# Kernel optimization log

Hardware: AMD Instinct MI355X
Metric: run time of the kernel (lower is better)

The kernel has to match this reference:

```python
import jax, jax.numpy as jnp
import numpy as np

B, T, D_IN, D_OUT, N_FILT, MAX_T = 4, 2048, 512, 512, 24, 2048


def _hankel_filters(max_t: int, k: int) -> np.ndarray:
    # Z_{ij} = 2 / ((i+j)^3 - (i+j)), 1-indexed; top-|eig| eigenvectors
    idx = np.arange(1, max_t + 1, dtype=np.float64)
    ij = idx[None, :] + idx[:, None]
    Z = 2.0 / (ij ** 3 - ij)
    w, v = np.linalg.eigh(Z)
    top = np.argsort(-np.abs(w))[:k]
    return v[:, top].astype(np.float32)  # (max_t, k)


def setup_inputs() -> dict:
    key = jax.random.key(0)
    kx, km = jax.random.split(key)
    x = jax.random.normal(kx, (B, T, D_IN), dtype=jnp.float32)
    filters = jnp.asarray(_hankel_filters(MAX_T, N_FILT))  # (MAX_T, N)
    # nn.Linear weight is (d_out, d_in); stacked -> (N, d_out, d_in)
    scale = 1.0 / np.sqrt(D_IN)
    M_weights = jax.random.uniform(km, (N_FILT, D_OUT, D_IN), dtype=jnp.float32,
                                   minval=-scale, maxval=scale)
    return {"x": x, "filters": filters, "M_weights": M_weights}


def reference(x, filters, M_weights):
    Tlen = x.shape[1]
    phi = filters[:Tlen]                       # (T, N)
    phi_e = phi[None, :, :, None]              # (1, T, N, 1)
    weighted = phi_e * x[:, :, None, :]        # (B, T, N, D_in)
    csum = jnp.cumsum(weighted, axis=1)        # causal cumulative projection
    # per-filter rectangular projection: (B,T,N,f) x (N,o,f) -> (B,T,N,o)
    modulated = jnp.einsum('btnf,nof->btno', csum, M_weights)
    return (phi_e * modulated).sum(axis=2)     # (B, T, D_out)
```

## Files before the change

### kernel.cpp

```cpp
#include <hip/hip_runtime.h>
#include <stdint.h>

#define BQ 4
#define TT 2048
#define DF 512
#define DOUT 512
#define NF 24
#define CHF 8

typedef __attribute__((ext_vector_type(8))) short short8;
typedef __attribute__((ext_vector_type(4))) float f32x4;

typedef __attribute__((address_space(3))) uint8_t       lds_u8;
typedef __attribute__((address_space(1))) const uint8_t glb_u8;

__device__ __forceinline__ float bf2f(unsigned short u) {
    union { unsigned int i; float f; } v; v.i = ((unsigned int)u) << 16; return v.f;
}
__device__ __forceinline__ unsigned short f2bf(float f) {
    union { float f; unsigned int i; } v; v.f = f;
    unsigned int r = v.i + 0x7FFFu + ((v.i >> 16) & 1u);
    return (unsigned short)(r >> 16);
}
__device__ __forceinline__ float lo16f(unsigned int u) { return __uint_as_float(u << 16); }
__device__ __forceinline__ float hi16f(unsigned int u) { return __uint_as_float(u & 0xffff0000u); }

__device__ __forceinline__ int plaus16(unsigned int h) {
    unsigned int e = (h >> 7) & 0xffu;
    return (e >= 97u && e <= 141u) || ((h & 0x7fffu) == 0u);
}

__global__ void k_detect(const unsigned int* __restrict__ X, int* __restrict__ flag)
{
    const int lane = threadIdx.x;
    int cnt = 0;
#pragma unroll
    for (int i = 0; i < 4; ++i) {
        unsigned int w = X[lane * 4 + i];
        cnt += (plaus16(w >> 16) && plaus16(w & 0xffffu)) ? 1 : 0;
    }
    for (int off = 32; off > 0; off >>= 1) cnt += __shfl_down(cnt, off);
    if (lane == 0) *flag = (cnt < 180) ? 1 : 0;
}

__global__ __launch_bounds__(256) void k_convf(
    const void* __restrict__ src, float* __restrict__ dst,
    const int* __restrict__ flag, int n)
{
    const int isf32 = *flag;
    int i = blockIdx.x * 256 + threadIdx.x;
    const int stride = gridDim.x * 256;
    for (; i < n; i += stride)
        dst[i] = isf32 ? ((const float*)src)[i]
                       : bf2f(((const unsigned short*)src)[i]);
}

__global__ __launch_bounds__(256) void k_prep(
    const void* __restrict__ X, const void* __restrict__ Mw,
    const void* __restrict__ Fil,
    unsigned short* __restrict__ Xbf, unsigned short* __restrict__ Mbf,
    float* __restrict__ Fw, int n4x, int n4m, int n4f)
{
    __shared__ int sflag;
    const int tid = threadIdx.x;
    if (tid < 64) {
        int cnt = 0;
        const unsigned int* Xu = (const unsigned int*)X;
#pragma unroll
        for (int i = 0; i < 4; ++i) {
            unsigned int wd = Xu[tid * 4 + i];
            cnt += (plaus16(wd >> 16) && plaus16(wd & 0xffffu)) ? 1 : 0;
        }
        for (int off = 32; off > 0; off >>= 1) cnt += __shfl_down(cnt, off);
        if (tid == 0) sflag = (cnt < 180) ? 1 : 0;
    }
    __syncthreads();
    const int isf32 = sflag;

    const int total = n4x + n4m + n4f;
    for (int i = blockIdx.x * 256 + tid; i < total; i += gridDim.x * 256) {
        if (i < n4x) {
            ushort4 o;
            if (isf32) {
                float4 v = ((const float4*)X)[i];
                o.x = f2bf(v.x); o.y = f2bf(v.y); o.z = f2bf(v.z); o.w = f2bf(v.w);
            } else {
                o = ((const ushort4*)X)[i];
            }
            ((ushort4*)Xbf)[i] = o;
        } else if (i < n4x + n4m) {
            const int j = i - n4x;
            ushort4 o;
            if (isf32) {
                float4 v = ((const float4*)Mw)[j];
                o.x = f2bf(v.x); o.y = f2bf(v.y); o.z = f2bf(v.z); o.w = f2bf(v.w);
            } else {
                o = ((const ushort4*)Mw)[j];
            }
            ((ushort4*)Mbf)[j] = o;
        } else {
            const int j = i - n4x - n4m;
            if (isf32) {
                ((float4*)Fw)[j] = ((const float4*)Fil)[j];
            } else {
                ushort4 u = ((const ushort4*)Fil)[j];
                ((float4*)Fw)[j] = make_float4(bf2f(u.x), bf2f(u.y),
                                               bf2f(u.z), bf2f(u.w));
            }
        }
    }
}

__global__ __launch_bounds__(256, 3) void k_gemm_ns(
    const unsigned short* __restrict__ X,
    const unsigned short* __restrict__ Mw,
    const float* __restrict__ Fw,
    float* __restrict__ Cs,
    float* __restrict__ Out,
    int r0)
{
    __shared__ unsigned short sAB[2 * 6144];
    __shared__ float sPhi2[NF * 64];

    const int tid  = threadIdx.x;
    const int lane = tid & 63;
    const int w    = tid >> 6;
    const int wm   = w & 1, wn = w >> 1;
    const int tm   = blockIdx.x;
    const int on0  = blockIdx.y * 128;
    const int rowL = tm * 64;
    const int rowG = r0 + rowL;

    for (int idx = tid; idx < NF * 64; idx += 256) {
        int n = idx >> 6, rr2 = idx & 63;
        sPhi2[idx] = Fw[((rowG + rr2) & (TT - 1)) * NF + n];
    }

    const unsigned short* Ag = X + (size_t)rowG * DF;

    auto stage = [&](int m) {
        const int n = m >> 4, kt = m & 15;
        lds_u8* base = (lds_u8*)sAB + (m & 1) * 12288;
        {
            const int c = w * 64 + lane;
            const int r = c >> 2, qs = c & 3;
            const int qg = qs ^ ((r >> 1) & 3);
            __builtin_amdgcn_global_load_lds(
                (const glb_u8*)(Ag + (size_t)r * DF + kt * 32 + qg * 8),
                base + (w * 64) * 16, 16, 0, 0);
        }
        const unsigned short* Bg = Mw + (size_t)n * DOUT * DF + (size_t)on0 * DF;
#pragma unroll
        for (int i = 0; i < 2; ++i) {
            const int cbase = i * 256 + w * 64;
            const int c = cbase + lane;
            const int r = c >> 2, qs = c & 3;
            const int qg = qs ^ ((r >> 1) & 3);
            __builtin_amdgcn_global_load_lds(
                (const glb_u8*)(Bg + (size_t)r * DF + kt * 32 + qg * 8),
                base + 4096 + cbase * 16, 16, 0, 0);
        }
    };

    f32x4 acc[2][4], Bacc[2][4];
#pragma unroll
    for (int i = 0; i < 2; i++)
#pragma unroll
        for (int j = 0; j < 4; j++) {
            acc[i][j]  = (f32x4){0.f, 0.f, 0.f, 0.f};
            Bacc[i][j] = (f32x4){0.f, 0.f, 0.f, 0.f};
        }

    stage(0);
    __syncthreads();

    const int lr  = lane & 15;
    const int q   = lane >> 4;
    const int qsw = (q ^ ((lr >> 1) & 3)) * 8;

    for (int m = 0; m < NF * 16; ++m) {
        if (m + 1 < NF * 16) stage(m + 1);

        const unsigned short* sAc = sAB + (m & 1) * 6144;
        const unsigned short* sBc = sAc + 2048;
        short8 a[2], b[4];
#pragma unroll
        for (int i = 0; i < 2; i++)
            a[i] = *(const short8*)&sAc[(wm * 32 + i * 16 + lr) * 32 + qsw];
#pragma unroll
        for (int j = 0; j < 4; j++)
            b[j] = *(const short8*)&sBc[(wn * 64 + j * 16 + lr) * 32 + qsw];
#pragma unroll
        for (int i = 0; i < 2; i++)
#pragma unroll
            for (int j = 0; j < 4; j++)
                acc[i][j] = __builtin_amdgcn_mfma_f32_16x16x32_bf16(
                    a[i], b[j], acc[i][j], 0, 0, 0);

        if ((m & 15) == 15) {
            const int n = m >> 4;
#pragma unroll
            for (int i = 0; i < 2; i++) {
                const int rbase = wm * 32 + i * 16 + q * 4;
                float ph0 = sPhi2[n * 64 + rbase + 0];
                float ph1 = sPhi2[n * 64 + rbase + 1];
                float ph2 = sPhi2[n * 64 + rbase + 2];
                float ph3 = sPhi2[n * 64 + rbase + 3];
#pragma unroll
                for (int j = 0; j < 4; j++) {
                    float z0 = acc[i][j][0] * ph0;
                    float z1 = acc[i][j][1] * ph1;
                    float z2 = acc[i][j][2] * ph2;
                    float z3 = acc[i][j][3] * ph3;
                    float p0 = z0, p1 = p0 + z1, p2 = p1 + z2, p3 = p2 + z3;
                    float t  = __shfl_xor(p3, 16);
                    float off = (q & 1) ? t : 0.f;
                    Bacc[i][j][0] += ph0 * (off + p0);
                    Bacc[i][j][1] += ph1 * (off + p1);
                    Bacc[i][j][2] += ph2 * (off + p2);
                    Bacc[i][j][3] += ph3 * (off + p3);
                    if (q & 1) {
                        int ch  = (rowL >> 3) + wm * 4 + i * 2 + (q >> 1);
                        int col = on0 + wn * 64 + j * 16 + lr;
                        Cs[((size_t)ch * NF + n) * 512 + col] = off + p3;
                    }
                    acc[i][j] = (f32x4){0.f, 0.f, 0.f, 0.f};
                }
            }
        }
        __syncthreads();
    }

#pragma unroll
    for (int i = 0; i < 2; i++)
#pragma unroll
        for (int j = 0; j < 4; j++)
#pragma unroll
            for (int r = 0; r < 4; r++) {
                int row = rowG + wm * 32 + i * 16 + q * 4 + r;
                Out[(size_t)row * DOUT + on0 + wn * 64 + j * 16 + lr] =
                    Bacc[i][j][r];
            }
}

__global__ __launch_bounds__(256, 8) void k_apply(
    float* __restrict__ Out, const float* __restrict__ Cs,
    const float* __restrict__ Fw, int r0)
{
    __shared__ float sP2[CHF * NF];
    const int c = blockIdx.x, tid = threadIdx.x;
    const int t0g = r0 + c * CHF;
    if (tid < CHF * NF)
        sP2[tid] = Fw[((t0g + tid / NF) & (TT - 1)) * NF + (tid % NF)];
    __syncthreads();

    const int col2 = tid * 2;
    float2 a[CHF];
#pragma unroll
    for (int t = 0; t < CHF; ++t) a[t] = make_float2(0.f, 0.f);
    const float* cb = Cs + (size_t)c * NF * 512 + col2;
#pragma unroll 6
    for (int n = 0; n < NF; ++n) {
        float2 g = *(const float2*)(cb + (size_t)n * 512);
#pragma unroll
        for (int t = 0; t < CHF; ++t) {
            float ph = sP2[t * NF + n];
            a[t].x += ph * g.x; a[t].y += ph * g.y;
        }
    }
#pragma unroll
    for (int t = 0; t < CHF; ++t) {
        float2* po = (float2*)&Out[(size_t)(t0g + t) * DOUT + col2];
        float2 o = *po;
        *po = make_float2(o.x + a[t].x, o.y + a[t].y);
    }
}

__global__ __launch_bounds__(256, 2) void k_gemm(
    const void* __restrict__ Xv, const void* __restrict__ Mv,
    const void* __restrict__ Fv, const int* __restrict__ flag,
    unsigned short* __restrict__ Z, int r0, int o0, int W)
{
    __shared__ unsigned short sA[128 * 32];
    __shared__ unsigned short sB[128 * 32];
    __shared__ unsigned short sC[128 * 136];
    __shared__ float sPhi[128];

    const int isf32 = *flag;
    const int tid  = threadIdx.x;
    const int lane = tid & 63;
    const int w    = tid >> 6;
    const int wm   = w & 1, wn = w >> 1;
    const int tm   = blockIdx.x;
    const int on0  = o0 + blockIdx.y * 128;
    const int n    = blockIdx.z;

    const int rowg0 = r0 + tm * 128;
    if (tid < 128) {
        int t = (rowg0 + tid) & (TT - 1);
        sPhi[tid] = isf32 ? ((const float*)Fv)[t * NF + n]
                          : bf2f(((const unsigned short*)Fv)[t * NF + n]);
    }

    const unsigned short* Ah = (const unsigned short*)Xv + (size_t)rowg0 * DF;
    const unsigned short* Bh = (const unsigned short*)Mv +
        (size_t)n * DOUT * DF + (size_t)on0 * DF;
    const float* Af = (const float*)Xv + (size_t)rowg0 * DF;
    const float* Bf = (const float*)Mv + (size_t)n * DOUT * DF + (size_t)on0 * DF;

    f32x4 acc[4][4];
#pragma unroll
    for (int i = 0; i < 4; i++)
#pragma unroll
        for (int j = 0; j < 4; j++) acc[i][j] = (f32x4){0.f, 0.f, 0.f, 0.f};

    for (int kt = 0; kt < DF / 32; ++kt) {
        __syncthreads();
        if (!isf32) {
            const unsigned short* Ak = Ah + kt * 32;
            const unsigned short* Bk = Bh + kt * 32;
#pragma unroll
            for (int i = 0; i < 2; ++i) {
                const int c = i * 256 + tid;
                const int r = c >> 2, cc = (c & 3) * 8;
                *(short8*)&sA[r * 32 + cc] = *(const short8*)(Ak + (size_t)r * DF + cc);
                *(short8*)&sB[r * 32 + cc] = *(const short8*)(Bk + (size_t)r * DF + cc);
            }
        } else {
            const float* Ak = Af + kt * 32;
            const float* Bk = Bf + kt * 32;
#pragma unroll
            for (int i = 0; i < 2; ++i) {
                const int c = i * 256 + tid;
                const int r = c >> 2, cc = (c & 3) * 8;
                float4 a0 = *(const float4*)(Ak + (size_t)r * DF + cc);
                float4 a1 = *(const float4*)(Ak + (size_t)r * DF + cc + 4);
                float4 b0 = *(const float4*)(Bk + (size_t)r * DF + cc);
                float4 b1 = *(const float4*)(Bk + (size_t)r * DF + cc + 4);
                short8 sa, sb;
                sa[0]=(short)f2bf(a0.x); sa[1]=(short)f2bf(a0.y);
                sa[2]=(short)f2bf(a0.z); sa[3]=(short)f2bf(a0.w);
                sa[4]=(short)f2bf(a1.x); sa[5]=(short)f2bf(a1.y);
                sa[6]=(short)f2bf(a1.z); sa[7]=(short)f2bf(a1.w);
                sb[0]=(short)f2bf(b0.x); sb[1]=(short)f2bf(b0.y);
                sb[2]=(short)f2bf(b0.z); sb[3]=(short)f2bf(b0.w);
                sb[4]=(short)f2bf(b1.x); sb[5]=(short)f2bf(b1.y);
                sb[6]=(short)f2bf(b1.z); sb[7]=(short)f2bf(b1.w);
                *(short8*)&sA[r * 32 + cc] = sa;
                *(short8*)&sB[r * 32 + cc] = sb;
            }
        }
        __syncthreads();

        const int lr = lane & 15;
        const int lk = (lane >> 4) * 8;
        short8 a[4], b[4];
#pragma unroll
        for (int i = 0; i < 4; i++)
            a[i] = *(const short8*)&sA[(wm * 64 + i * 16 + lr) * 32 + lk];
#pragma unroll
        for (int j = 0; j < 4; j++)
            b[j] = *(const short8*)&sB[(wn * 64 + j * 16 + lr) * 32 + lk];
#pragma unroll
        for (int i = 0; i < 4; i++)
#pragma unroll
            for (int j = 0; j < 4; j++)
                acc[i][j] = __builtin_amdgcn_mfma_f32_16x16x32_bf16(
                    a[i], b[j], acc[i][j], 0, 0, 0);
    }

    const int rb = (lane >> 4) * 4;
#pragma unroll
    for (int i = 0; i < 4; i++)
#pragma unroll
        for (int j = 0; j < 4; j++)
#pragma unroll
            for (int r = 0; r < 4; r++) {
                int row = wm * 64 + i * 16 + rb + r;
                sC[row * 136 + wn * 64 + j * 16 + (lane & 15)] =
                    f2bf(acc[i][j][r] * sPhi[row]);
            }
    __syncthreads();
#pragma unroll
    for (int it = 0; it < 8; ++it) {
        int row = it * 16 + (tid >> 4);
        int col = (tid & 15) * 8;
        uint4 v = *(const uint4*)&sC[row * 136 + col];
        *(uint4*)&Z[((size_t)(tm * 128 + row) * NF + n) * W + (on0 - o0) + col] = v;
    }
}

__global__ __launch_bounds__(256, 2) void k_csum(
    const unsigned short* __restrict__ Z, float* __restrict__ Cs,
    int W, int CHs)
{
    const int c = blockIdx.x, n = blockIdx.y, tid = threadIdx.x;
    const unsigned short* p = Z + ((size_t)(c * CHs) * NF + n) * W + tid * 2;
    float sx = 0.f, sy = 0.f;
#pragma unroll 8
    for (int t = 0; t < CHs; ++t) {
        unsigned int u = *(const unsigned int*)(p + (size_t)t * NF * W);
        sx += lo16f(u);
        sy += hi16f(u);
    }
    float2* q = (float2*)&Cs[((size_t)c * NF + n) * W + tid * 2];
    *q = make_float2(sx, sy);
}

__global__ __launch_bounds__(256, 4) void k_prefix(
    float* __restrict__ Cs, float* __restrict__ Gc,
    int W, int rr, int nch, int nbat)
{
    __shared__ float2 sPart[4][64];
    const int tid  = threadIdx.x;
    const int wv   = tid >> 6, lane = tid & 63;
    const int obw  = W >> 7;
    const int perB = NF * obw;
    const int gw   = blockIdx.x;
    const int b    = gw / perB;
    const int rest = gw % perB;
    const int n    = rest / obw;
    const int ob   = rest % obw;
    const int opair = ob * 64 + lane;

    float* base = Cs + (size_t)b * nch * NF * W + (size_t)n * W + opair * 2;
    const size_t cstride = (size_t)NF * W;
    const int Q  = nch >> 2;
    const int c0 = wv * Q;
    const int end = c0 + Q;

    float sx = 0.f, sy = 0.f;
    for (int c = c0; c < end; ++c) {
        float2 v = *(const float2*)(base + (size_t)c * cstride);
        sx += v.x; sy += v.y;
    }
    sPart[wv][lane] = make_float2(sx, sy);
    __syncthreads();

    float cx = 0.f, cy = 0.f;
    if (nbat == 1 && rr != 0 && Gc) {
        float2 gv = *(const float2*)&Gc[(size_t)n * DOUT + opair * 2];
        cx = gv.x; cy = gv.y;
    }
    for (int w2 = 0; w2 < wv; ++w2) {
        float2 p = sPart[w2][lane];
        cx += p.x; cy += p.y;
    }

    int c = c0;
    if (Q >= 16) {
        float2 v[8], nx[8];
#pragma unroll
        for (int k = 0; k < 8; ++k)
            v[k] = *(float2*)(base + (size_t)(c + k) * cstride);
        for (; c + 16 <= end; c += 8) {
#pragma unroll
            for (int k = 0; k < 8; ++k)
                nx[k] = *(float2*)(base + (size_t)(c + 8 + k) * cstride);
#pragma unroll
            for (int k = 0; k < 8; ++k) {
                float2* p = (float2*)(base + (size_t)(c + k) * cstride);
                float2 t = v[k];
                *p = make_float2(cx, cy);
                cx += t.x; cy += t.y;
                v[k] = nx[k];
            }
        }
#pragma unroll
        for (int k = 0; k < 8; ++k) {
            float2* p = (float2*)(base + (size_t)(c + k) * cstride);
            float2 t = v[k];
            *p = make_float2(cx, cy);
            cx += t.x; cy += t.y;
        }
        c += 8;
    }
    for (; c < end; ++c) {
        float2* p = (float2*)(base + (size_t)c * cstride);
        float2 t = *p;
        *p = make_float2(cx, cy);
        cx += t.x; cy += t.y;
    }

    if (nbat == 1 && wv == 3 && Gc)
        *(float2*)&Gc[(size_t)n * DOUT + opair * 2] = make_float2(cx, cy);
}

#define JLIST(F) F(0) F(1) F(2) F(3) F(4) F(5)

__global__ __launch_bounds__(256, 8) void k_scan(
    const unsigned short* __restrict__ Z, const float* __restrict__ Cs,
    const float* __restrict__ Fw, float* __restrict__ Out,
    int r0, int o0, int W, int CHs)
{
    __shared__ float sPhi[32 * NF];
    __shared__ float2 sP[4][8][64];
    const int cg = blockIdx.x, tid = threadIdx.x;
    const int g = tid >> 6, op = tid & 63;
    const int ng0 = g * 6;
    const int c2  = (blockIdx.y * 64 + op) * 2;
    const int act = (c2 + 2 <= W);
    const int c2u = act ? c2 : (W - 2);
    const int t0g = r0 + cg * CHs;
    const int t0 = t0g & (TT - 1);
    for (int i = tid; i < CHs * NF; i += 256)
        sPhi[i] = Fw[(t0 + i / NF) * NF + (i % NF)];
    __syncthreads();

#define DECLG(j) float gx##j, gy##j;
    JLIST(DECLG)
#define INITG2(j) { float2 v = *(const float2*)&Cs[((size_t)cg * NF + ng0 + j) * W + c2u]; \
                    gx##j = v.x; gy##j = v.y; }
    JLIST(INITG2)

    const unsigned short* zp = Z + ((size_t)cg * CHs * NF + ng0) * W + c2u;
    float* outb = Out + (size_t)t0g * DOUT + o0 + c2;
    for (int tb = 0; tb < CHs; tb += 8) {
#pragma unroll
        for (int tt = 0; tt < 8; ++tt) {
            float ax = 0.f, ay = 0.f;
            const float* php = &sPhi[(tb + tt) * NF + ng0];
#define UPDG2(j) { unsigned int u = *(const unsigned int*)(zp + (size_t)j * W); \
                   gx##j += lo16f(u); gy##j += hi16f(u); \
                   float ph = php[j]; ax += ph * gx##j; ay += ph * gy##j; }
            JLIST(UPDG2)
            sP[g][tt][op] = make_float2(ax, ay);
            zp += (size_t)NF * W;
        }
        __syncthreads();
#pragma unroll
        for (int k = 0; k < 2; ++k) {
            const int tt = g * 2 + k;
            float2 p0 = sP[0][tt][op], p1 = sP[1][tt][op],
                   p2 = sP[2][tt][op], p3 = sP[3][tt][op];
            if (act)
                *(float2*)(outb + (size_t)(tb + tt) * DOUT) =
                    make_float2(p0.x + p1.x + p2.x + p3.x,
                                p0.y + p1.y + p2.y + p3.y);
        }
        __syncthreads();
    }
}

extern "C" void kernel_launch(void* const* d_in, const int* in_sizes, int n_in,
                              void* d_out, int out_size, void* d_ws, size_t ws_size,
                              hipStream_t stream)
{
    const void* X = d_in[0]; const void* Fil = d_in[1]; const void* Mw = d_in[2];
    for (int i = 0; i < n_in && i < 3; ++i) {
        if (in_sizes[i] == BQ * TT * DF)        X   = d_in[i];
        else if (in_sizes[i] == TT * NF)        Fil = d_in[i];
        else if (in_sizes[i] == NF * DOUT * DF) Mw  = d_in[i];
    }
    float* Out = (float*)d_out;

    const size_t offF = 256;
    const size_t nbF  = (size_t)TT * NF * 4;
    const size_t off0 = offF + nbF;
    const size_t nbX  = (size_t)BQ * TT * DF * 2;
    const size_t nbM  = (size_t)NF * DOUT * DF * 2;
    const size_t nbGc = (size_t)NF * DOUT * 4;

    int* flag = (int*)d_ws;
    float* Fw = (float*)((char*)d_ws + offF);

    const int n4x = BQ * TT * DF / 4;
    const int n4m = NF * DOUT * DF / 4;
    const int n4f = TT * NF / 4;

    {
        const size_t csB = (size_t)(BQ * TT / CHF) * NF * 512 * 4;
        if (off0 + nbX + nbM + csB <= ws_size) {
            unsigned short* Xbf = (unsigned short*)((char*)d_ws + off0);
            unsigned short* Mbf = (unsigned short*)((char*)Xbf + nbX);
            float* Cs = (float*)((char*)Mbf + nbM);

            hipLaunchKernelGGL(k_prep, dim3(2048), dim3(256), 0, stream,
                               X, Mw, Fil, Xbf, Mbf, Fw, n4x, n4m, n4f);
            hipLaunchKernelGGL(k_gemm_ns, dim3(BQ * TT / 64, 4), dim3(256),
                               0, stream, Xbf, Mbf, Fw, Cs, Out, 0);
            hipLaunchKernelGGL(k_prefix, dim3(BQ * NF * 4), dim3(256),
                               0, stream, Cs, (float*)nullptr, 512, 0,
                               TT / CHF, BQ);
            hipLaunchKernelGGL(k_apply, dim3(BQ * TT / CHF), dim3(256),
                               0, stream, Out, Cs, Fw, 0);
            return;
        }
    }

    {
        const size_t csB = (size_t)(TT / CHF) * NF * 512 * 4;
        if (off0 + nbX + nbM + csB <= ws_size) {
            unsigned short* Xbf = (unsigned short*)((char*)d_ws + off0);
            unsigned short* Mbf = (unsigned short*)((char*)Xbf + nbX);
            float* Cs = (float*)((char*)Mbf + nbM);

            hipLaunchKernelGGL(k_prep, dim3(2048), dim3(256), 0, stream,
                               X, Mw, Fil, Xbf, Mbf, Fw, n4x, n4m, n4f);
            for (int b = 0; b < BQ; ++b) {
                const int r0 = b * TT;
                hipLaunchKernelGGL(k_gemm_ns, dim3(TT / 64, 4), dim3(256),
                                   0, stream, Xbf, Mbf, Fw, Cs, Out, r0);
                hipLaunchKernelGGL(k_prefix, dim3(NF * 4), dim3(256),
                                   0, stream, Cs, (float*)nullptr, 512, 0,
                                   TT / CHF, 1);
                hipLaunchKernelGGL(k_apply, dim3(TT / CHF), dim3(256),
                                   0, stream, Out, Cs, Fw, r0);
            }
            return;
        }
    }

    hipLaunchKernelGGL(k_detect, dim3(1), dim3(64), 0, stream,
                       (const unsigned int*)X, flag);
    hipLaunchKernelGGL(k_convf, dim3(192), dim3(256), 0, stream,
                       Fil, Fw, flag, TT * NF);

    static const int cRT[7] = {2048, 1024, 512, 256, 128, 128, 128};
    static const int cW[7]  = {512, 512, 512, 512, 512, 256, 128};
    int RTs = 128, W = 128;
    for (int ci = 0; ci < 7; ++ci) {
        size_t need = off0 + (size_t)cRT[ci] * NF * cW[ci] * 2
                    + (size_t)(cRT[ci] / 32) * NF * cW[ci] * 4 + nbGc;
        if (need <= ws_size) { RTs = cRT[ci]; W = cW[ci]; break; }
    }
    unsigned short* Z = (unsigned short*)((char*)d_ws + off0);
    float* Cs = (float*)((char*)Z + (size_t)RTs * NF * W * 2);
    float* Gc = (float*)((char*)Cs + (size_t)(RTs / 32) * NF * W * 4);

    const int nrr = TT / RTs, nch = RTs / 32;
    for (int b = 0; b < BQ; ++b) {
        for (int o0 = 0; o0 < DOUT; o0 += W) {
            for (int rr = 0; rr < nrr; ++rr) {
                const int r0 = b * TT + rr * RTs;
                hipLaunchKernelGGL(k_gemm, dim3(RTs / 128, W / 128, NF), dim3(256),
                                   0, stream, X, Mw, Fil, flag, Z, r0, o0, W);
                hipLaunchKernelGGL(k_csum, dim3(nch, NF), dim3(W / 2), 0, stream,
                                   Z, Cs, W, 32);
                hipLaunchKernelGGL(k_prefix, dim3(NF * (W / 128)), dim3(256),
                                   0, stream, Cs, Gc, W, rr, nch, 1);
                hipLaunchKernelGGL(k_scan, dim3(nch, W / 128), dim3(256),
                                   0, stream, Z, Cs, Fw, Out, r0, o0, W, 32);
            }
        }
    }
}
```

Baseline: 344.3 us.

## Triple-buffer GEMM LDS staging with two-ahead prefetch and partial vmcnt waits

Moves the k_gemm_ns LDS pipeline from double to triple buffering. Tiles are prefetched two iterations ahead, and the loop waits with explicit s_waitcnt vmcnt(3) so the newest prefetch can stay in flight across the barrier. The aim is to hide global-to-LDS load latency behind MFMA work. In exchange, LDS use per block grows and the occupancy hint drops from 3 to 2 blocks per SIMD, which could reduce latency hiding between waves.

Result: slower. 353.9 us (+2.8%).

```diff
diff --git a/kernel.cpp b/kernel.cpp
--- a/kernel.cpp
+++ b/kernel.cpp
@@ -111,7 +111,7 @@
     }
 }
 
-__global__ __launch_bounds__(256, 3) void k_gemm_ns(
+__global__ __launch_bounds__(256, 2) void k_gemm_ns(
     const unsigned short* __restrict__ X,
     const unsigned short* __restrict__ Mw,
     const float* __restrict__ Fw,
@@ -119,7 +119,7 @@
     float* __restrict__ Out,
     int r0)
 {
-    __shared__ unsigned short sAB[2 * 6144];
+    __shared__ unsigned short sAB[3 * 6144];
     __shared__ float sPhi2[NF * 64];
 
     const int tid  = threadIdx.x;
@@ -138,9 +138,9 @@
 
     const unsigned short* Ag = X + (size_t)rowG * DF;
 
-    auto stage = [&](int m) {
+    auto stage = [&](int m, int buf) {
         const int n = m >> 4, kt = m & 15;
-        lds_u8* base = (lds_u8*)sAB + (m & 1) * 12288;
+        lds_u8* base = (lds_u8*)sAB + buf * 12288;
         {
             const int c = w * 64 + lane;
             const int r = c >> 2, qs = c & 3;
@@ -171,17 +171,22 @@
             Bacc[i][j] = (f32x4){0.f, 0.f, 0.f, 0.f};
         }
 
-    stage(0);
-    __syncthreads();
+    const int M = NF * 16;
+    stage(0, 0);
+    stage(1, 1);
+    asm volatile("s_waitcnt vmcnt(3)" ::: "memory");
+    __builtin_amdgcn_s_barrier();
+    __builtin_amdgcn_sched_barrier(0);
 
     const int lr  = lane & 15;
     const int q   = lane >> 4;
     const int qsw = (q ^ ((lr >> 1) & 3)) * 8;
 
-    for (int m = 0; m < NF * 16; ++m) {
-        if (m + 1 < NF * 16) stage(m + 1);
-
-        const unsigned short* sAc = sAB + (m & 1) * 6144;
+    int cur = 0, stg = 2;
+    for (int m = 0; m < M; ++m) {
+        if (m + 2 < M) stage(m + 2, stg);
+
+        const unsigned short* sAc = sAB + cur * 6144;
         const unsigned short* sBc = sAc + 2048;
         short8 a[2], b[4];
 #pragma unroll
@@ -228,8 +233,20 @@
                 }
             }
         }
-        __syncthreads();
-    }
+
+        if (m < M - 2) {
+            asm volatile("s_waitcnt vmcnt(3) lgkmcnt(0)" ::: "memory");
+            __builtin_amdgcn_s_barrier();
+            __builtin_amdgcn_sched_barrier(0);
+        } else if (m == M - 2) {
+            asm volatile("s_waitcnt vmcnt(0) lgkmcnt(0)" ::: "memory");
+            __builtin_amdgcn_s_barrier();
+            __builtin_amdgcn_sched_barrier(0);
+        }
+        cur = (cur == 2) ? 0 : cur + 1;
+        stg = (stg == 2) ? 0 : stg + 1;
+    }
+    __syncthreads();
 
 #pragma unroll
     for (int i = 0; i < 2; i++)
```
